# Kernel optimization log

Measured on AMD Instinct MI355X. Metric: run time of the kernel, lower is better.

## Reference

```python
import jax, jax.numpy as jnp
import numpy as np

B, T, H = 1024, 256, 128

def _gru(x, Wx, Wh, b):
    # Keras GRU (reset_after=True), gate order z, r, h. x: [B,T,D], b: [2,3H]
    xp = x @ Wx + b[0]                      # [B,T,3H]
    h0 = jnp.zeros((x.shape[0], Wh.shape[0]), x.dtype)
    def step(h, xt):
        hp = h @ Wh + b[1]
        xz, xr, xh = jnp.split(xt, 3, axis=-1)
        hz, hr, hn = jnp.split(hp, 3, axis=-1)
        z = jax.nn.sigmoid(xz + hz)
        r = jax.nn.sigmoid(xr + hr)
        hh = jnp.tanh(xh + r * hn)
        return z * h + (1.0 - z) * hh, None
    h, _ = jax.lax.scan(step, h0, jnp.swapaxes(xp, 0, 1))
    return h                                 # [B,H]

def setup_inputs() -> dict:
    key = jax.random.key(0)
    ks = jax.random.split(key, 32)
    def gp(k, shape, scale=0.05):
        return (jax.random.normal(k, shape, dtype=jnp.float32) * scale)
    inp = {
        "spatial": jax.random.normal(ks[0], (B, T, 2), dtype=jnp.float32),
        "hour_idx": jax.random.randint(ks[1], (B, T), 0, 24, dtype=jnp.int32),
        "week_idx": jax.random.randint(ks[2], (B, T), 0, 7, dtype=jnp.int32),
        "E_time": gp(ks[3], (24, H)),
        "E_week": gp(ks[4], (7, H)),
        # spatial GRU (input dim 2)
        "Ws_x": gp(ks[5], (2, 3 * H)), "Ws_h": gp(ks[6], (H, 3 * H)), "bs": gp(ks[7], (2, 3 * H)),
        # hour temporal GRU (input dim 128)
        "Wh_x": gp(ks[8], (H, 3 * H)), "Wh_h": gp(ks[9], (H, 3 * H)), "bh": gp(ks[10], (2, 3 * H)),
        # week temporal GRU (input dim 128)
        "Ww_x": gp(ks[11], (H, 3 * H)), "Ww_h": gp(ks[12], (H, 3 * H)), "bw": gp(ks[13], (2, 3 * H)),
        # attention Dense(3) over the channel axis of size 3
        "Wa": gp(ks[14], (3, 3)), "ba": gp(ks[15], (3,)),
        # MLP
        "W1": gp(ks[16], (H, 1024)), "b1": gp(ks[17], (1024,)),
        "W2": gp(ks[18], (1024, 512)), "b2": gp(ks[19], (512,)),
        "W3": gp(ks[20], (512, 256)), "b3": gp(ks[21], (256,)),
        "W4": gp(ks[22], (256, H)), "b4": gp(ks[23], (H,)),
        "Wo": gp(ks[24], (H, 1)), "bo": gp(ks[25], (1,)),
    }
    return inp

def reference(spatial, hour_idx, week_idx, E_time, E_week,
              Ws_x, Ws_h, bs, Wh_x, Wh_h, bh, Ww_x, Ww_h, bw,
              Wa, ba, W1, b1, W2, b2, W3, b3, W4, b4, Wo, bo):
    te = E_time[hour_idx]                    # [B,T,128] gather
    we = E_week[week_idx]                    # [B,T,128] gather
    fs = _gru(spatial, Ws_x, Ws_h, bs)       # [B,128]
    fh = _gru(te, Wh_x, Wh_h, bh)            # [B,128]
    fw = _gru(we, Ww_x, Ww_h, bw)            # [B,128]
    allf = jnp.stack([fs, fh, fw], axis=-1)  # [B,128,3]
    scores = jax.nn.softmax(jax.nn.relu(allf @ Wa + ba), axis=-1)
    sf = jnp.sum(allf * scores, axis=-1)     # [B,128] attention-fused features
    x = jax.nn.relu(sf @ W1 + b1)
    x = jax.nn.relu(x @ W2 + b2)
    x = jax.nn.relu(x @ W3 + b3)
    x = jax.nn.relu(x @ W4 + b4)
    out = (x + sf) @ Wo + bo                 # residual then Dense(1)
    return out[:, 0]                         # [B]
```

## Files before the change

### kernel.cpp

```cpp
#include <hip/hip_runtime.h>
#include <hip/hip_bf16.h>

typedef __attribute__((ext_vector_type(8))) short short8;
typedef __attribute__((ext_vector_type(4))) float f32x4;
typedef __attribute__((ext_vector_type(2))) float f32x2;

#define LOG2E  1.44269504088896340736f
#define NLOG2E (-1.44269504088896340736f)
#define TLOG2E (2.88539008177792681472f)

__device__ __forceinline__ unsigned short f2bf(float f) {
  unsigned u = __builtin_bit_cast(unsigned, f);
  u += 0x7fffu + ((u >> 16) & 1u);
  return (unsigned short)(u >> 16);
}

__global__ void setup_kernel(
    const float* __restrict__ E_time, const float* __restrict__ E_week,
    const float* __restrict__ Wh_x, const float* __restrict__ bh,
    const float* __restrict__ Ww_x, const float* __restrict__ bw,
    const float* __restrict__ W1, const float* __restrict__ W2,
    const float* __restrict__ W3, const float* __restrict__ W4,
    float* __restrict__ Ptime, float* __restrict__ Pweek,
    unsigned short* __restrict__ Wt)
{
  const int b = blockIdx.x;
  const int tid = threadIdx.x;
  if (b < 31) {
    const int c = tid;
    if (b < 24) {
      float acc = bh[c];
      for (int d = 0; d < 128; ++d)
        acc = fmaf(E_time[b * 128 + d], Wh_x[d * 384 + c], acc);
      Ptime[b * 384 + c] = acc;
    } else {
      const int r = b - 24;
      float acc = bw[c];
      for (int d = 0; d < 128; ++d)
        acc = fmaf(E_week[r * 128 + d], Ww_x[d * 384 + c], acc);
      Pweek[r * 384 + c] = acc;
    }
    return;
  }
  const int id = (b - 31) * 384 + tid;
  if (id >= 819200) return;
  if (id < 131072) {
    const int n = id >> 7, k = id & 127;
    Wt[id] = f2bf(W1[k * 1024 + n]);
  } else if (id < 655360) {
    const int off = id - 131072, n = off >> 10, k = off & 1023;
    Wt[id] = f2bf(W2[k * 512 + n]);
  } else if (id < 786432) {
    const int off = id - 655360, n = off >> 9, k = off & 511;
    Wt[id] = f2bf(W3[k * 256 + n]);
  } else {
    const int off = id - 786432, n = off >> 8, k = off & 255;
    Wt[id] = f2bf(W4[k * 128 + n]);
  }
}

__global__ __launch_bounds__(512) void gru_kernel(
    const float* __restrict__ spatial,
    const int* __restrict__ hour_idx,
    const int* __restrict__ week_idx,
    const float* __restrict__ Ws_x,
    const float* __restrict__ Ws_h, const float* __restrict__ bs,
    const float* __restrict__ Wh_h, const float* __restrict__ bh,
    const float* __restrict__ Ww_h, const float* __restrict__ bw,
    const float* __restrict__ Ptime, const float* __restrict__ Pweek,
    float* __restrict__ fs, float* __restrict__ fh, float* __restrict__ fw)
{
  __shared__ __align__(16) unsigned short h_bf[2][16 * 136];
  __shared__ __align__(16) float ptab3[24 * 387 + 1];
  __shared__ __align__(16) float xsp[256 * 16 * 2];
  __shared__ __align__(16) unsigned char idx8[256 * 16];

  const int tid  = threadIdx.x;
  const int lane = tid & 63;
  const int wv   = tid >> 6;
  const int ar   = lane & 15;
  const int akg  = lane >> 4;
  const int gid  = blockIdx.x;
  const int gru  = gid >> 6;
  const int row0 = (gid & 63) * 16;

  const float* __restrict__ Wh   = (gru == 0) ? Ws_h : (gru == 1) ? Wh_h : Ww_h;
  const float* __restrict__ bvec = (gru == 0) ? bs   : (gru == 1) ? bh   : bw;
  float* __restrict__ fout       = (gru == 0) ? fs   : (gru == 1) ? fh   : fw;

  const int j = wv * 16 + ar;
  const float gsc[3] = {NLOG2E, NLOG2E, TLOG2E};

  short8 wfrag[3][4];
  #pragma unroll
  for (int g = 0; g < 3; ++g) {
    const int n = g * 128 + j;
    #pragma unroll
    for (int ks = 0; ks < 4; ++ks) {
      const int k0 = ks * 32 + akg * 8;
      short8 f;
      #pragma unroll
      for (int q = 0; q < 8; ++q)
        f[q] = (short)f2bf(Wh[(k0 + q) * 384 + n] * gsc[g]);
      wfrag[g][ks] = f;
    }
  }

  const float bz = bvec[384 +       j] * NLOG2E;
  const float br = bvec[384 + 128 + j] * NLOG2E;
  const float bn = bvec[384 + 256 + j] * TLOG2E;

  float w0g[3] = {0, 0, 0}, w1g[3] = {0, 0, 0}, b0g[3] = {0, 0, 0};
  if (gru == 0) {
    #pragma unroll
    for (int g = 0; g < 3; ++g) {
      w0g[g] = Ws_x[      g * 128 + j] * gsc[g];
      w1g[g] = Ws_x[384 + g * 128 + j] * gsc[g];
      b0g[g] = bvec[      g * 128 + j] * gsc[g];
    }
  }

  if (gru == 0) {
    for (int e = tid; e < 16 * 256; e += 512) {
      const int i = e >> 8, t = e & 255;
      const f32x2 v = *(const f32x2*)&spatial[((row0 + i) * 256 + t) * 2];
      *(f32x2*)&xsp[(t * 16 + i) * 2] = v;
    }
  } else {
    const int* __restrict__ idxg = (gru == 1) ? hour_idx : week_idx;
    for (int e = tid; e < 16 * 256; e += 512) {
      const int i = e >> 8, t = e & 255;
      idx8[t * 16 + i] = (unsigned char)idxg[(row0 + i) * 256 + t];
    }
    const float* __restrict__ P = (gru == 1) ? Ptime : Pweek;
    const int nr = (gru == 1) ? 24 : 7;
    for (int e = tid; e < nr * 384; e += 512) {
      const int ix = e / 384, c = e - ix * 384;
      const int g = c >> 7, jj = c & 127;
      ptab3[ix * 387 + jj * 3 + g] = P[e] * gsc[g];
    }
  }
  for (int e = tid; e < 16 * 136; e += 512) h_bf[0][e] = 0;

  auto loadx = [&](int t, float (&xp)[4][3]) {
    if (gru == 0) {
      #pragma unroll
      for (int r2 = 0; r2 < 4; ++r2) {
        const f32x2 s = *(const f32x2*)&xsp[(t * 16 + akg * 4 + r2) * 2];
        #pragma unroll
        for (int g = 0; g < 3; ++g)
          xp[r2][g] = fmaf(s.y, w1g[g], fmaf(s.x, w0g[g], b0g[g]));
      }
    } else {
      const unsigned pk = *(const unsigned*)&idx8[t * 16 + akg * 4];
      #pragma unroll
      for (int r2 = 0; r2 < 4; ++r2) {
        const int ix = (pk >> (8 * r2)) & 255;
        const float* __restrict__ p = &ptab3[ix * 387 + j * 3];
        xp[r2][0] = p[0]; xp[r2][1] = p[1]; xp[r2][2] = p[2];
      }
    }
  };

  __syncthreads();

  float hst[4] = {0.f, 0.f, 0.f, 0.f};
  float xpc[4][3];
  loadx(0, xpc);
  int cur = 0;

  #pragma unroll 2
  for (int t = 0; t < 256; ++t) {
    f32x4 accz = {bz, bz, bz, bz};
    f32x4 accr = {br, br, br, br};
    f32x4 accn = {bn, bn, bn, bn};
    const unsigned short* __restrict__ hb = h_bf[cur];
    #pragma unroll
    for (int ks = 0; ks < 4; ++ks) {
      const short8 a = *(const short8*)&hb[ar * 136 + ks * 32 + akg * 8];
      accz = __builtin_amdgcn_mfma_f32_16x16x32_bf16(a, wfrag[0][ks], accz, 0, 0, 0);
      accr = __builtin_amdgcn_mfma_f32_16x16x32_bf16(a, wfrag[1][ks], accr, 0, 0, 0);
      accn = __builtin_amdgcn_mfma_f32_16x16x32_bf16(a, wfrag[2][ks], accn, 0, 0, 0);
    }

    float xpn[4][3];
    if (t < 255) loadx(t + 1, xpn);

    float hn4[4];
    #pragma unroll
    for (int r2 = 0; r2 < 4; ++r2) {
      const float z  = __builtin_amdgcn_rcpf(1.f + __builtin_amdgcn_exp2f(xpc[r2][0] + accz[r2]));
      const float rr = __builtin_amdgcn_rcpf(1.f + __builtin_amdgcn_exp2f(xpc[r2][1] + accr[r2]));
      const float e  = __builtin_amdgcn_exp2f(fmaf(rr, accn[r2], xpc[r2][2]));
      const float hh = fmaf(-2.f, __builtin_amdgcn_rcpf(e + 1.f), 1.f);
      hn4[r2] = fmaf(z, hst[r2] - hh, hh);
      hst[r2] = hn4[r2];
    }

    unsigned p01, p23;
    asm("v_cvt_pk_bf16_f32 %0, %1, %2" : "=v"(p01) : "v"(hn4[0]), "v"(hn4[1]));
    asm("v_cvt_pk_bf16_f32 %0, %1, %2" : "=v"(p23) : "v"(hn4[2]), "v"(hn4[3]));
    unsigned short* __restrict__ ho = h_bf[cur ^ 1];
    ho[(akg * 4 + 0) * 136 + j] = (unsigned short)(p01 & 0xffffu);
    ho[(akg * 4 + 1) * 136 + j] = (unsigned short)(p01 >> 16);
    ho[(akg * 4 + 2) * 136 + j] = (unsigned short)(p23 & 0xffffu);
    ho[(akg * 4 + 3) * 136 + j] = (unsigned short)(p23 >> 16);

    __syncthreads();
    cur ^= 1;
    #pragma unroll
    for (int r2 = 0; r2 < 4; ++r2) {
      xpc[r2][0] = xpn[r2][0]; xpc[r2][1] = xpn[r2][1]; xpc[r2][2] = xpn[r2][2];
    }
  }

  #pragma unroll
  for (int r2 = 0; r2 < 4; ++r2)
    fout[(row0 + akg * 4 + r2) * 128 + j] = hst[r2];
}

template<int K, int N>
__device__ __forceinline__ void mlp_layer(
    const unsigned short* __restrict__ xin, unsigned short* __restrict__ xout,
    const unsigned short* __restrict__ Wt, const float* __restrict__ bias,
    int lane, int wv, float* __restrict__ foutF)
{
  constexpr int NT = N / 64;
  const int ar  = lane & 15;
  const int akg = lane >> 4;
  f32x4 acc[NT];
  #pragma unroll
  for (int nt = 0; nt < NT; ++nt) acc[nt] = f32x4{0.f, 0.f, 0.f, 0.f};
  for (int ks = 0; ks < K / 32; ++ks) {
    const short8 a = *(const short8*)&xin[ar * 1032 + ks * 32 + akg * 8];
    #pragma unroll
    for (int nt = 0; nt < NT; ++nt) {
      const int n = wv * (N / 4) + nt * 16 + ar;
      const short8 b = *(const short8*)&Wt[n * K + ks * 32 + akg * 8];
      acc[nt] = __builtin_amdgcn_mfma_f32_16x16x32_bf16(a, b, acc[nt], 0, 0, 0);
    }
  }
  const int rbase = akg * 4;
  #pragma unroll
  for (int nt = 0; nt < NT; ++nt) {
    const int n = wv * (N / 4) + nt * 16 + ar;
    const float bv = bias[n];
    #pragma unroll
    for (int q = 0; q < 4; ++q) {
      float v = acc[nt][q] + bv;
      v = fmaxf(v, 0.f);
      xout[(rbase + q) * 1032 + n] = f2bf(v);
      if (foutF) foutF[(rbase + q) * 128 + n] = v;
    }
  }
}

__global__ __launch_bounds__(256) void attn_mlp_kernel(
    const float* __restrict__ fs, const float* __restrict__ fh, const float* __restrict__ fw,
    const float* __restrict__ Wa, const float* __restrict__ ba,
    const unsigned short* __restrict__ Wt,
    const float* __restrict__ b1, const float* __restrict__ b2,
    const float* __restrict__ b3, const float* __restrict__ b4,
    const float* __restrict__ Wo, const float* __restrict__ bo,
    float* __restrict__ out)
{
  __shared__ __align__(16) unsigned short xa[16 * 1032];
  __shared__ __align__(16) unsigned short xb[16 * 1032];
  __shared__ __align__(16) float sf_l[16 * 128];
  __shared__ __align__(16) float x4f[16 * 128];

  const int tid  = threadIdx.x;
  const int lane = tid & 63;
  const int wv   = tid >> 6;
  const int row0 = blockIdx.x * 16;

  {
    const int i  = tid >> 4;
    const int j0 = (tid & 15) * 8;
    float wa[9], bav[3];
    #pragma unroll
    for (int q = 0; q < 9; ++q) wa[q] = Wa[q];
    #pragma unroll
    for (int q = 0; q < 3; ++q) bav[q] = ba[q];
    const int base = (row0 + i) * 128 + j0;
    #pragma unroll
    for (int half = 0; half < 2; ++half) {
      const f32x4 a = *(const f32x4*)&fs[base + half * 4];
      const f32x4 b = *(const f32x4*)&fh[base + half * 4];
      const f32x4 c = *(const f32x4*)&fw[base + half * 4];
      #pragma unroll
      for (int q = 0; q < 4; ++q) {
        const float f0 = a[q], f1 = b[q], f2 = c[q];
        float s0 = f0 * wa[0] + f1 * wa[3] + f2 * wa[6] + bav[0];
        float s1 = f0 * wa[1] + f1 * wa[4] + f2 * wa[7] + bav[1];
        float s2 = f0 * wa[2] + f1 * wa[5] + f2 * wa[8] + bav[2];
        s0 = fmaxf(s0, 0.f); s1 = fmaxf(s1, 0.f); s2 = fmaxf(s2, 0.f);
        const float m  = fmaxf(s0, fmaxf(s1, s2));
        const float e0 = __builtin_amdgcn_exp2f((s0 - m) * LOG2E);
        const float e1 = __builtin_amdgcn_exp2f((s1 - m) * LOG2E);
        const float e2 = __builtin_amdgcn_exp2f((s2 - m) * LOG2E);
        const float inv = __builtin_amdgcn_rcpf(e0 + e1 + e2);
        const float sf  = (f0 * e0 + f1 * e1 + f2 * e2) * inv;
        const int jj = j0 + half * 4 + q;
        sf_l[i * 128 + jj] = sf;
        xa[i * 1032 + jj]  = f2bf(sf);
      }
    }
  }
  __syncthreads();

  mlp_layer<128, 1024>(xa, xb, Wt,          b1, lane, wv, nullptr);
  __syncthreads();
  mlp_layer<1024, 512>(xb, xa, Wt + 131072, b2, lane, wv, nullptr);
  __syncthreads();
  mlp_layer<512,  256>(xa, xb, Wt + 655360, b3, lane, wv, nullptr);
  __syncthreads();
  mlp_layer<256,  128>(xb, xa, Wt + 786432, b4, lane, wv, x4f);
  __syncthreads();

  const int row = tid >> 4;
  const int p   = tid & 15;
  float part = 0.f;
  #pragma unroll
  for (int q = 0; q < 8; ++q) {
    const int jj = p + q * 16;
    part += (x4f[row * 128 + jj] + sf_l[row * 128 + jj]) * Wo[jj];
  }
  #pragma unroll
  for (int off = 8; off > 0; off >>= 1)
    part += __shfl_xor(part, off, 16);
  if (p == 0) out[row0 + row] = part + bo[0];
}

extern "C" void kernel_launch(void* const* d_in, const int* in_sizes, int n_in,
                              void* d_out, int out_size, void* d_ws, size_t ws_size,
                              hipStream_t stream) {
  const float* spatial  = (const float*)d_in[0];
  const int*   hour_idx = (const int*)d_in[1];
  const int*   week_idx = (const int*)d_in[2];
  const float* E_time   = (const float*)d_in[3];
  const float* E_week   = (const float*)d_in[4];
  const float* Ws_x = (const float*)d_in[5];
  const float* Ws_h = (const float*)d_in[6];
  const float* bs   = (const float*)d_in[7];
  const float* Wh_x = (const float*)d_in[8];
  const float* Wh_h = (const float*)d_in[9];
  const float* bh   = (const float*)d_in[10];
  const float* Ww_x = (const float*)d_in[11];
  const float* Ww_h = (const float*)d_in[12];
  const float* bw   = (const float*)d_in[13];
  const float* Wa   = (const float*)d_in[14];
  const float* ba   = (const float*)d_in[15];
  const float* W1   = (const float*)d_in[16];
  const float* b1   = (const float*)d_in[17];
  const float* W2   = (const float*)d_in[18];
  const float* b2   = (const float*)d_in[19];
  const float* W3   = (const float*)d_in[20];
  const float* b3   = (const float*)d_in[21];
  const float* W4   = (const float*)d_in[22];
  const float* b4   = (const float*)d_in[23];
  const float* Wo   = (const float*)d_in[24];
  const float* bo   = (const float*)d_in[25];
  float* out = (float*)d_out;

  float* ws    = (float*)d_ws;
  float* Ptime = ws;
  float* Pweek = Ptime + 9216;
  float* fsb   = Pweek + 2688;
  float* fhb   = fsb + 131072;
  float* fwb   = fhb + 131072;
  unsigned short* Wt = (unsigned short*)(fwb + 131072);

  setup_kernel<<<31 + 2134, 384, 0, stream>>>(E_time, E_week, Wh_x, bh, Ww_x, bw,
      W1, W2, W3, W4, Ptime, Pweek, Wt);
  gru_kernel<<<192, 512, 0, stream>>>(spatial, hour_idx, week_idx, Ws_x,
      Ws_h, bs, Wh_h, bh, Ww_h, bw, Ptime, Pweek, fsb, fhb, fwb);
  attn_mlp_kernel<<<64, 256, 0, stream>>>(fsb, fhb, fwb, Wa, ba, Wt,
      b1, b2, b3, b4, Wo, bo, out);
}
```

Measured before the change: 264.4 us.

## Halve GRU block to 4 waves each owning two hidden-column tiles

```diff
diff --git a/kernel.cpp b/kernel.cpp
--- a/kernel.cpp
+++ b/kernel.cpp
@@ -8,6 +8,9 @@
 #define LOG2E  1.44269504088896340736f
 #define NLOG2E (-1.44269504088896340736f)
 #define TLOG2E (2.88539008177792681472f)
+
+#define HS 152
+#define PS 524
 
 __device__ __forceinline__ unsigned short f2bf(float f) {
   unsigned u = __builtin_bit_cast(unsigned, f);
@@ -59,7 +62,7 @@
   }
 }
 
-__global__ __launch_bounds__(512) void gru_kernel(
+__global__ __launch_bounds__(256, 1) void gru_kernel(
     const float* __restrict__ spatial,
     const int* __restrict__ hour_idx,
     const int* __restrict__ week_idx,
@@ -70,8 +73,8 @@
     const float* __restrict__ Ptime, const float* __restrict__ Pweek,
     float* __restrict__ fs, float* __restrict__ fh, float* __restrict__ fw)
 {
-  __shared__ __align__(16) unsigned short h_bf[2][16 * 136];
-  __shared__ __align__(16) float ptab3[24 * 387 + 1];
+  __shared__ __align__(16) unsigned short h_bf[2][16 * HS];
+  __shared__ __align__(16) float ptab4[24 * PS];
   __shared__ __align__(16) float xsp[256 * 16 * 2];
   __shared__ __align__(16) unsigned char idx8[256 * 16];
 
@@ -88,135 +91,157 @@
   const float* __restrict__ bvec = (gru == 0) ? bs   : (gru == 1) ? bh   : bw;
   float* __restrict__ fout       = (gru == 0) ? fs   : (gru == 1) ? fh   : fw;
 
-  const int j = wv * 16 + ar;
+  const int j1 = wv * 16 + ar;
+  const int j2 = j1 + 64;
   const float gsc[3] = {NLOG2E, NLOG2E, TLOG2E};
 
-  short8 wfrag[3][4];
+  short8 wfrag[3][2][4];
   #pragma unroll
   for (int g = 0; g < 3; ++g) {
-    const int n = g * 128 + j;
-    #pragma unroll
-    for (int ks = 0; ks < 4; ++ks) {
-      const int k0 = ks * 32 + akg * 8;
-      short8 f;
-      #pragma unroll
-      for (int q = 0; q < 8; ++q)
-        f[q] = (short)f2bf(Wh[(k0 + q) * 384 + n] * gsc[g]);
-      wfrag[g][ks] = f;
-    }
-  }
-
-  const float bz = bvec[384 +       j] * NLOG2E;
-  const float br = bvec[384 + 128 + j] * NLOG2E;
-  const float bn = bvec[384 + 256 + j] * TLOG2E;
-
-  float w0g[3] = {0, 0, 0}, w1g[3] = {0, 0, 0}, b0g[3] = {0, 0, 0};
+    #pragma unroll
+    for (int jh = 0; jh < 2; ++jh) {
+      const int n = g * 128 + jh * 64 + j1;
+      #pragma unroll
+      for (int ks = 0; ks < 4; ++ks) {
+        const int k0 = ks * 32 + akg * 8;
+        short8 f;
+        #pragma unroll
+        for (int q = 0; q < 8; ++q)
+          f[q] = (short)f2bf(Wh[(k0 + q) * 384 + n] * gsc[g]);
+        wfrag[g][jh][ks] = f;
+      }
+    }
+  }
+
+  float bacc[3][2];
+  #pragma unroll
+  for (int g = 0; g < 3; ++g) {
+    bacc[g][0] = bvec[384 + g * 128 + j1] * gsc[g];
+    bacc[g][1] = bvec[384 + g * 128 + j2] * gsc[g];
+  }
+
+  float w0g[2][3], w1g[2][3], b0g[2][3];
   if (gru == 0) {
     #pragma unroll
-    for (int g = 0; g < 3; ++g) {
-      w0g[g] = Ws_x[      g * 128 + j] * gsc[g];
-      w1g[g] = Ws_x[384 + g * 128 + j] * gsc[g];
-      b0g[g] = bvec[      g * 128 + j] * gsc[g];
+    for (int jh = 0; jh < 2; ++jh) {
+      const int jj = jh ? j2 : j1;
+      #pragma unroll
+      for (int g = 0; g < 3; ++g) {
+        w0g[jh][g] = Ws_x[      g * 128 + jj] * gsc[g];
+        w1g[jh][g] = Ws_x[384 + g * 128 + jj] * gsc[g];
+        b0g[jh][g] = bvec[      g * 128 + jj] * gsc[g];
+      }
     }
   }
 
   if (gru == 0) {
-    for (int e = tid; e < 16 * 256; e += 512) {
+    for (int e = tid; e < 16 * 256; e += 256) {
       const int i = e >> 8, t = e & 255;
       const f32x2 v = *(const f32x2*)&spatial[((row0 + i) * 256 + t) * 2];
       *(f32x2*)&xsp[(t * 16 + i) * 2] = v;
     }
   } else {
     const int* __restrict__ idxg = (gru == 1) ? hour_idx : week_idx;
-    for (int e = tid; e < 16 * 256; e += 512) {
+    for (int e = tid; e < 16 * 256; e += 256) {
       const int i = e >> 8, t = e & 255;
       idx8[t * 16 + i] = (unsigned char)idxg[(row0 + i) * 256 + t];
     }
     const float* __restrict__ P = (gru == 1) ? Ptime : Pweek;
     const int nr = (gru == 1) ? 24 : 7;
-    for (int e = tid; e < nr * 384; e += 512) {
+    for (int e = tid; e < nr * 384; e += 256) {
       const int ix = e / 384, c = e - ix * 384;
       const int g = c >> 7, jj = c & 127;
-      ptab3[ix * 387 + jj * 3 + g] = P[e] * gsc[g];
-    }
-  }
-  for (int e = tid; e < 16 * 136; e += 512) h_bf[0][e] = 0;
-
-  auto loadx = [&](int t, float (&xp)[4][3]) {
+      ptab4[ix * PS + jj * 4 + g] = P[e] * gsc[g];
+    }
+  }
+  for (int e = tid; e < 16 * HS; e += 256) h_bf[0][e] = 0;
+  __syncthreads();
+
+  float hst[2][4];
+  #pragma unroll
+  for (int jh = 0; jh < 2; ++jh)
+    #pragma unroll
+    for (int r2 = 0; r2 < 4; ++r2) hst[jh][r2] = 0.f;
+
+  const int abase = ar * HS;
+
+  auto step = [&](int t, const unsigned short* __restrict__ hb,
+                  unsigned short* __restrict__ ho) {
+    float xp[4][2][3];
     if (gru == 0) {
       #pragma unroll
       for (int r2 = 0; r2 < 4; ++r2) {
         const f32x2 s = *(const f32x2*)&xsp[(t * 16 + akg * 4 + r2) * 2];
         #pragma unroll
-        for (int g = 0; g < 3; ++g)
-          xp[r2][g] = fmaf(s.y, w1g[g], fmaf(s.x, w0g[g], b0g[g]));
+        for (int jh = 0; jh < 2; ++jh)
+          #pragma unroll
+          for (int g = 0; g < 3; ++g)
+            xp[r2][jh][g] = fmaf(s.y, w1g[jh][g], fmaf(s.x, w0g[jh][g], b0g[jh][g]));
       }
     } else {
       const unsigned pk = *(const unsigned*)&idx8[t * 16 + akg * 4];
       #pragma unroll
       for (int r2 = 0; r2 < 4; ++r2) {
         const int ix = (pk >> (8 * r2)) & 255;
-        const float* __restrict__ p = &ptab3[ix * 387 + j * 3];
-        xp[r2][0] = p[0]; xp[r2][1] = p[1]; xp[r2][2] = p[2];
-      }
-    }
+        const f32x4 v1 = *(const f32x4*)&ptab4[ix * PS + j1 * 4];
+        const f32x4 v2 = *(const f32x4*)&ptab4[ix * PS + j2 * 4];
+        xp[r2][0][0] = v1.x; xp[r2][0][1] = v1.y; xp[r2][0][2] = v1.z;
+        xp[r2][1][0] = v2.x; xp[r2][1][1] = v2.y; xp[r2][1][2] = v2.z;
+      }
+    }
+
+    f32x4 acc[3][2];
+    #pragma unroll
+    for (int g = 0; g < 3; ++g)
+      #pragma unroll
+      for (int jh = 0; jh < 2; ++jh)
+        acc[g][jh] = f32x4{bacc[g][jh], bacc[g][jh], bacc[g][jh], bacc[g][jh]};
+    #pragma unroll
+    for (int ks = 0; ks < 4; ++ks) {
+      const short8 a = *(const short8*)&hb[abase + ks * 32 + akg * 8];
+      #pragma unroll
+      for (int g = 0; g < 3; ++g)
+        #pragma unroll
+        for (int jh = 0; jh < 2; ++jh)
+          acc[g][jh] = __builtin_amdgcn_mfma_f32_16x16x32_bf16(a, wfrag[g][jh][ks], acc[g][jh], 0, 0, 0);
+    }
+
+    #pragma unroll
+    for (int jh = 0; jh < 2; ++jh) {
+      float hn4[4];
+      #pragma unroll
+      for (int r2 = 0; r2 < 4; ++r2) {
+        const float z  = __builtin_amdgcn_rcpf(1.f + __builtin_amdgcn_exp2f(xp[r2][jh][0] + acc[0][jh][r2]));
+        const float rr = __builtin_amdgcn_rcpf(1.f + __builtin_amdgcn_exp2f(xp[r2][jh][1] + acc[1][jh][r2]));
+        const float e  = __builtin_amdgcn_exp2f(fmaf(rr, acc[2][jh][r2], xp[r2][jh][2]));
+        const float hh = fmaf(-2.f, __builtin_amdgcn_rcpf(e + 1.f), 1.f);
+        hn4[r2] = fmaf(z, hst[jh][r2] - hh, hh);
+        hst[jh][r2] = hn4[r2];
+      }
+      unsigned p01, p23;
+      asm("v_cvt_pk_bf16_f32 %0, %1, %2" : "=v"(p01) : "v"(hn4[0]), "v"(hn4[1]));
+      asm("v_cvt_pk_bf16_f32 %0, %1, %2" : "=v"(p23) : "v"(hn4[2]), "v"(hn4[3]));
+      const int jj = jh ? j2 : j1;
+      ho[(akg * 4 + 0) * HS + jj] = (unsigned short)(p01 & 0xffffu);
+      ho[(akg * 4 + 1) * HS + jj] = (unsigned short)(p01 >> 16);
+      ho[(akg * 4 + 2) * HS + jj] = (unsigned short)(p23 & 0xffffu);
+      ho[(akg * 4 + 3) * HS + jj] = (unsigned short)(p23 >> 16);
+    }
+    __syncthreads();
   };
 
-  __syncthreads();
-
-  float hst[4] = {0.f, 0.f, 0.f, 0.f};
-  float xpc[4][3];
-  loadx(0, xpc);
-  int cur = 0;
-
-  #pragma unroll 2
-  for (int t = 0; t < 256; ++t) {
-    f32x4 accz = {bz, bz, bz, bz};
-    f32x4 accr = {br, br, br, br};
-    f32x4 accn = {bn, bn, bn, bn};
-    const unsigned short* __restrict__ hb = h_bf[cur];
-    #pragma unroll
-    for (int ks = 0; ks < 4; ++ks) {
-      const short8 a = *(const short8*)&hb[ar * 136 + ks * 32 + akg * 8];
-      accz = __builtin_amdgcn_mfma_f32_16x16x32_bf16(a, wfrag[0][ks], accz, 0, 0, 0);
-      accr = __builtin_amdgcn_mfma_f32_16x16x32_bf16(a, wfrag[1][ks], accr, 0, 0, 0);
-      accn = __builtin_amdgcn_mfma_f32_16x16x32_bf16(a, wfrag[2][ks], accn, 0, 0, 0);
-    }
-
-    float xpn[4][3];
-    if (t < 255) loadx(t + 1, xpn);
-
-    float hn4[4];
-    #pragma unroll
-    for (int r2 = 0; r2 < 4; ++r2) {
-      const float z  = __builtin_amdgcn_rcpf(1.f + __builtin_amdgcn_exp2f(xpc[r2][0] + accz[r2]));
-      const float rr = __builtin_amdgcn_rcpf(1.f + __builtin_amdgcn_exp2f(xpc[r2][1] + accr[r2]));
-      const float e  = __builtin_amdgcn_exp2f(fmaf(rr, accn[r2], xpc[r2][2]));
-      const float hh = fmaf(-2.f, __builtin_amdgcn_rcpf(e + 1.f), 1.f);
-      hn4[r2] = fmaf(z, hst[r2] - hh, hh);
-      hst[r2] = hn4[r2];
-    }
-
-    unsigned p01, p23;
-    asm("v_cvt_pk_bf16_f32 %0, %1, %2" : "=v"(p01) : "v"(hn4[0]), "v"(hn4[1]));
-    asm("v_cvt_pk_bf16_f32 %0, %1, %2" : "=v"(p23) : "v"(hn4[2]), "v"(hn4[3]));
-    unsigned short* __restrict__ ho = h_bf[cur ^ 1];
-    ho[(akg * 4 + 0) * 136 + j] = (unsigned short)(p01 & 0xffffu);
-    ho[(akg * 4 + 1) * 136 + j] = (unsigned short)(p01 >> 16);
-    ho[(akg * 4 + 2) * 136 + j] = (unsigned short)(p23 & 0xffffu);
-    ho[(akg * 4 + 3) * 136 + j] = (unsigned short)(p23 >> 16);
-
-    __syncthreads();
-    cur ^= 1;
-    #pragma unroll
-    for (int r2 = 0; r2 < 4; ++r2) {
-      xpc[r2][0] = xpn[r2][0]; xpc[r2][1] = xpn[r2][1]; xpc[r2][2] = xpn[r2][2];
-    }
-  }
-
-  #pragma unroll
-  for (int r2 = 0; r2 < 4; ++r2)
-    fout[(row0 + akg * 4 + r2) * 128 + j] = hst[r2];
+  for (int tt = 0; tt < 128; ++tt) {
+    step(2 * tt,     h_bf[0], h_bf[1]);
+    step(2 * tt + 1, h_bf[1], h_bf[0]);
+  }
+
+  #pragma unroll
+  for (int jh = 0; jh < 2; ++jh) {
+    const int jj = jh ? j2 : j1;
+    #pragma unroll
+    for (int r2 = 0; r2 < 4; ++r2)
+      fout[(row0 + akg * 4 + r2) * 128 + jj] = hst[jh][r2];
+  }
 }
 
 template<int K, int N>
@@ -373,7 +398,7 @@
 
   setup_kernel<<<31 + 2134, 384, 0, stream>>>(E_time, E_week, Wh_x, bh, Ww_x, bw,
       W1, W2, W3, W4, Ptime, Pweek, Wt);
-  gru_kernel<<<192, 512, 0, stream>>>(spatial, hour_idx, week_idx, Ws_x,
+  gru_kernel<<<192, 256, 0, stream>>>(spatial, hour_idx, week_idx, Ws_x,
       Ws_h, bs, Wh_h, bh, Ww_h, bw, Ptime, Pweek, fsb, fhb, fwb);
   attn_mlp_kernel<<<64, 256, 0, stream>>>(fsb, fhb, fwb, Wa, ba, Wt,
       b1, b2, b3, b4, Wo, bo, out);
```

Measured after the change: 277.7 us. +5.0%, slower.

## Fold GRU input projection into recurrent MFMA via augmented one-hot K slice

Applied to the files above, without the earlier changes.

```diff
diff --git a/kernel.cpp b/kernel.cpp
--- a/kernel.cpp
+++ b/kernel.cpp
@@ -8,6 +8,8 @@
 #define LOG2E  1.44269504088896340736f
 #define NLOG2E (-1.44269504088896340736f)
 #define TLOG2E (2.88539008177792681472f)
+
+#define HES 168
 
 __device__ __forceinline__ unsigned short f2bf(float f) {
   unsigned u = __builtin_bit_cast(unsigned, f);
@@ -59,7 +61,7 @@
   }
 }
 
-__global__ __launch_bounds__(512) void gru_kernel(
+__global__ __launch_bounds__(512, 2) void gru_kernel(
     const float* __restrict__ spatial,
     const int* __restrict__ hour_idx,
     const int* __restrict__ week_idx,
@@ -70,10 +72,7 @@
     const float* __restrict__ Ptime, const float* __restrict__ Pweek,
     float* __restrict__ fs, float* __restrict__ fh, float* __restrict__ fw)
 {
-  __shared__ __align__(16) unsigned short h_bf[2][16 * 136];
-  __shared__ __align__(16) float ptab3[24 * 387 + 1];
-  __shared__ __align__(16) float xsp[256 * 16 * 2];
-  __shared__ __align__(16) unsigned char idx8[256 * 16];
+  __shared__ __align__(16) unsigned short hx[2][16 * HES];
 
   const int tid  = threadIdx.x;
   const int lane = tid & 63;
@@ -87,136 +86,148 @@
   const float* __restrict__ Wh   = (gru == 0) ? Ws_h : (gru == 1) ? Wh_h : Ww_h;
   const float* __restrict__ bvec = (gru == 0) ? bs   : (gru == 1) ? bh   : bw;
   float* __restrict__ fout       = (gru == 0) ? fs   : (gru == 1) ? fh   : fw;
+  const float* __restrict__ Ptab = (gru == 1) ? Ptime : Pweek;
+  const int* __restrict__ idxg   = (gru == 1) ? hour_idx : week_idx;
+  const int NR = (gru == 1) ? 24 : 7;
 
   const int j = wv * 16 + ar;
-  const float gsc[3] = {NLOG2E, NLOG2E, TLOG2E};
-
-  short8 wfrag[3][4];
-  #pragma unroll
-  for (int g = 0; g < 3; ++g) {
-    const int n = g * 128 + j;
-    #pragma unroll
-    for (int ks = 0; ks < 4; ++ks) {
-      const int k0 = ks * 32 + akg * 8;
+
+  short8 wf[15];
+  #pragma unroll
+  for (int g = 0; g < 2; ++g) {
+    #pragma unroll
+    for (int ks = 0; ks < 5; ++ks) {
       short8 f;
       #pragma unroll
-      for (int q = 0; q < 8; ++q)
-        f[q] = (short)f2bf(Wh[(k0 + q) * 384 + n] * gsc[g]);
-      wfrag[g][ks] = f;
-    }
-  }
-
-  const float bz = bvec[384 +       j] * NLOG2E;
-  const float br = bvec[384 + 128 + j] * NLOG2E;
-  const float bn = bvec[384 + 256 + j] * TLOG2E;
-
-  float w0g[3] = {0, 0, 0}, w1g[3] = {0, 0, 0}, b0g[3] = {0, 0, 0};
-  if (gru == 0) {
-    #pragma unroll
-    for (int g = 0; g < 3; ++g) {
-      w0g[g] = Ws_x[      g * 128 + j] * gsc[g];
-      w1g[g] = Ws_x[384 + g * 128 + j] * gsc[g];
-      b0g[g] = bvec[      g * 128 + j] * gsc[g];
-    }
-  }
-
-  if (gru == 0) {
-    for (int e = tid; e < 16 * 256; e += 512) {
-      const int i = e >> 8, t = e & 255;
-      const f32x2 v = *(const f32x2*)&spatial[((row0 + i) * 256 + t) * 2];
-      *(f32x2*)&xsp[(t * 16 + i) * 2] = v;
-    }
-  } else {
-    const int* __restrict__ idxg = (gru == 1) ? hour_idx : week_idx;
-    for (int e = tid; e < 16 * 256; e += 512) {
-      const int i = e >> 8, t = e & 255;
-      idx8[t * 16 + i] = (unsigned char)idxg[(row0 + i) * 256 + t];
-    }
-    const float* __restrict__ P = (gru == 1) ? Ptime : Pweek;
-    const int nr = (gru == 1) ? 24 : 7;
-    for (int e = tid; e < nr * 384; e += 512) {
-      const int ix = e / 384, c = e - ix * 384;
-      const int g = c >> 7, jj = c & 127;
-      ptab3[ix * 387 + jj * 3 + g] = P[e] * gsc[g];
-    }
-  }
-  for (int e = tid; e < 16 * 136; e += 512) h_bf[0][e] = 0;
-
-  auto loadx = [&](int t, float (&xp)[4][3]) {
+      for (int q = 0; q < 8; ++q) {
+        const int k = ks * 32 + akg * 8 + q;
+        float v;
+        if (k < 128) v = Wh[k * 384 + g * 128 + j];
+        else {
+          const int p = k - 128;
+          if (gru == 0) v = (p == 0) ? Ws_x[g * 128 + j]
+                          : (p == 1) ? Ws_x[384 + g * 128 + j] : 0.f;
+          else          v = (p < NR) ? Ptab[p * 384 + g * 128 + j] : 0.f;
+        }
+        f[q] = (short)f2bf(v * NLOG2E);
+      }
+      wf[g * 5 + ks] = f;
+    }
+  }
+  #pragma unroll
+  for (int ks = 0; ks < 4; ++ks) {
+    short8 f;
+    #pragma unroll
+    for (int q = 0; q < 8; ++q) {
+      const int k = ks * 32 + akg * 8 + q;
+      f[q] = (short)f2bf(Wh[k * 384 + 256 + j] * TLOG2E);
+    }
+    wf[10 + ks] = f;
+  }
+  {
+    short8 f;
+    #pragma unroll
+    for (int q = 0; q < 8; ++q) {
+      const int p = akg * 8 + q;
+      float v;
+      if (gru == 0) v = (p == 0) ? Ws_x[256 + j]
+                      : (p == 1) ? Ws_x[384 + 256 + j] : 0.f;
+      else          v = (p < NR) ? Ptab[p * 384 + 256 + j] : 0.f;
+      f[q] = (short)f2bf(v * TLOG2E);
+    }
+    wf[14] = f;
+  }
+
+  const float bz  = (bvec[384 + j]       + (gru == 0 ? bvec[j]       : 0.f)) * NLOG2E;
+  const float br  = (bvec[384 + 128 + j] + (gru == 0 ? bvec[128 + j] : 0.f)) * NLOG2E;
+  const float bnh = bvec[384 + 256 + j] * TLOG2E;
+  const float bnx = (gru == 0 ? bvec[256 + j] : 0.f) * TLOG2E;
+
+  for (int e = tid; e < 2 * 16 * HES; e += 512) ((unsigned short*)hx)[e] = 0;
+  __syncthreads();
+
+  const bool mt  = (tid & 31) == 0;
+  const int mrow = tid >> 5;
+  int ix_prev = 0, ix_cur = 0;
+  if (mt) {
     if (gru == 0) {
-      #pragma unroll
-      for (int r2 = 0; r2 < 4; ++r2) {
-        const f32x2 s = *(const f32x2*)&xsp[(t * 16 + akg * 4 + r2) * 2];
-        #pragma unroll
-        for (int g = 0; g < 3; ++g)
-          xp[r2][g] = fmaf(s.y, w1g[g], fmaf(s.x, w0g[g], b0g[g]));
+      const f32x2 s = *(const f32x2*)&spatial[(row0 + mrow) * 512];
+      unsigned pk;
+      asm("v_cvt_pk_bf16_f32 %0, %1, %2" : "=v"(pk) : "v"(s.x), "v"(s.y));
+      *(unsigned*)&hx[0][mrow * HES + 128] = pk;
+    } else {
+      ix_cur = idxg[(row0 + mrow) * 256];
+      hx[0][mrow * HES + 128 + ix_cur] = 0x3F80;
+    }
+  }
+  __syncthreads();
+
+  float hst[4] = {0.f, 0.f, 0.f, 0.f};
+
+  for (int t = 0; t < 256; ++t) {
+    const unsigned short* __restrict__ hb = hx[t & 1];
+    unsigned short* __restrict__ ho       = hx[(t + 1) & 1];
+
+    short8 a[5];
+    #pragma unroll
+    for (int ks = 0; ks < 5; ++ks)
+      a[ks] = *(const short8*)&hb[ar * HES + ks * 32 + akg * 8];
+
+    f32x2 msp = {0.f, 0.f};
+    int ix_next = 0;
+    const bool mact = mt && (t + 1 < 256);
+    if (mact) {
+      if (gru == 0) msp = *(const f32x2*)&spatial[(row0 + mrow) * 512 + 2 * (t + 1)];
+      else          ix_next = idxg[(row0 + mrow) * 256 + t + 1];
+    }
+
+    f32x4 az  = {bz, bz, bz, bz};
+    f32x4 arr = {br, br, br, br};
+    f32x4 anh = {bnh, bnh, bnh, bnh};
+    f32x4 anx = {bnx, bnx, bnx, bnx};
+    #pragma unroll
+    for (int ks = 0; ks < 4; ++ks) {
+      az  = __builtin_amdgcn_mfma_f32_16x16x32_bf16(a[ks], wf[ks],      az,  0, 0, 0);
+      arr = __builtin_amdgcn_mfma_f32_16x16x32_bf16(a[ks], wf[5 + ks],  arr, 0, 0, 0);
+      anh = __builtin_amdgcn_mfma_f32_16x16x32_bf16(a[ks], wf[10 + ks], anh, 0, 0, 0);
+    }
+    az  = __builtin_amdgcn_mfma_f32_16x16x32_bf16(a[4], wf[4],  az,  0, 0, 0);
+    arr = __builtin_amdgcn_mfma_f32_16x16x32_bf16(a[4], wf[9],  arr, 0, 0, 0);
+    anx = __builtin_amdgcn_mfma_f32_16x16x32_bf16(a[4], wf[14], anx, 0, 0, 0);
+
+    if (mact) {
+      if (gru == 0) {
+        unsigned pk;
+        asm("v_cvt_pk_bf16_f32 %0, %1, %2" : "=v"(pk) : "v"(msp.x), "v"(msp.y));
+        *(unsigned*)&ho[mrow * HES + 128] = pk;
+      } else {
+        if (t >= 1) ho[mrow * HES + 128 + ix_prev] = 0;
+        ho[mrow * HES + 128 + ix_next] = 0x3F80;
+        ix_prev = ix_cur; ix_cur = ix_next;
       }
-    } else {
-      const unsigned pk = *(const unsigned*)&idx8[t * 16 + akg * 4];
-      #pragma unroll
-      for (int r2 = 0; r2 < 4; ++r2) {
-        const int ix = (pk >> (8 * r2)) & 255;
-        const float* __restrict__ p = &ptab3[ix * 387 + j * 3];
-        xp[r2][0] = p[0]; xp[r2][1] = p[1]; xp[r2][2] = p[2];
-      }
-    }
-  };
-
-  __syncthreads();
-
-  float hst[4] = {0.f, 0.f, 0.f, 0.f};
-  float xpc[4][3];
-  loadx(0, xpc);
-  int cur = 0;
-
-  #pragma unroll 2
-  for (int t = 0; t < 256; ++t) {
-    f32x4 accz = {bz, bz, bz, bz};
-    f32x4 accr = {br, br, br, br};
-    f32x4 accn = {bn, bn, bn, bn};
-    const unsigned short* __restrict__ hb = h_bf[cur];
-    #pragma unroll
-    for (int ks = 0; ks < 4; ++ks) {
-      const short8 a = *(const short8*)&hb[ar * 136 + ks * 32 + akg * 8];
-      accz = __builtin_amdgcn_mfma_f32_16x16x32_bf16(a, wfrag[0][ks], accz, 0, 0, 0);
-      accr = __builtin_amdgcn_mfma_f32_16x16x32_bf16(a, wfrag[1][ks], accr, 0, 0, 0);
-      accn = __builtin_amdgcn_mfma_f32_16x16x32_bf16(a, wfrag[2][ks], accn, 0, 0, 0);
-    }
-
-    float xpn[4][3];
-    if (t < 255) loadx(t + 1, xpn);
+    }
 
     float hn4[4];
     #pragma unroll
-    for (int r2 = 0; r2 < 4; ++r2) {
-      const float z  = __builtin_amdgcn_rcpf(1.f + __builtin_amdgcn_exp2f(xpc[r2][0] + accz[r2]));
-      const float rr = __builtin_amdgcn_rcpf(1.f + __builtin_amdgcn_exp2f(xpc[r2][1] + accr[r2]));
-      const float e  = __builtin_amdgcn_exp2f(fmaf(rr, accn[r2], xpc[r2][2]));
+    for (int q = 0; q < 4; ++q) {
+      const float z  = __builtin_amdgcn_rcpf(1.f + __builtin_amdgcn_exp2f(az[q]));
+      const float r  = __builtin_amdgcn_rcpf(1.f + __builtin_amdgcn_exp2f(arr[q]));
+      const float e  = __builtin_amdgcn_exp2f(fmaf(r, anh[q], anx[q]));
       const float hh = fmaf(-2.f, __builtin_amdgcn_rcpf(e + 1.f), 1.f);
-      hn4[r2] = fmaf(z, hst[r2] - hh, hh);
-      hst[r2] = hn4[r2];
-    }
-
-    unsigned p01, p23;
-    asm("v_cvt_pk_bf16_f32 %0, %1, %2" : "=v"(p01) : "v"(hn4[0]), "v"(hn4[1]));
-    asm("v_cvt_pk_bf16_f32 %0, %1, %2" : "=v"(p23) : "v"(hn4[2]), "v"(hn4[3]));
-    unsigned short* __restrict__ ho = h_bf[cur ^ 1];
-    ho[(akg * 4 + 0) * 136 + j] = (unsigned short)(p01 & 0xffffu);
-    ho[(akg * 4 + 1) * 136 + j] = (unsigned short)(p01 >> 16);
-    ho[(akg * 4 + 2) * 136 + j] = (unsigned short)(p23 & 0xffffu);
-    ho[(akg * 4 + 3) * 136 + j] = (unsigned short)(p23 >> 16);
+      hn4[q] = fmaf(z, hst[q] - hh, hh);
+      hst[q] = hn4[q];
+    }
+
+    #pragma unroll
+    for (int q = 0; q < 4; ++q)
+      ho[(akg * 4 + q) * HES + j] = f2bf(hn4[q]);
 
     __syncthreads();
-    cur ^= 1;
-    #pragma unroll
-    for (int r2 = 0; r2 < 4; ++r2) {
-      xpc[r2][0] = xpn[r2][0]; xpc[r2][1] = xpn[r2][1]; xpc[r2][2] = xpn[r2][2];
-    }
-  }
-
-  #pragma unroll
-  for (int r2 = 0; r2 < 4; ++r2)
-    fout[(row0 + akg * 4 + r2) * 128 + j] = hst[r2];
+  }
+
+  #pragma unroll
+  for (int q = 0; q < 4; ++q)
+    fout[(row0 + akg * 4 + q) * 128 + j] = hst[q];
 }
 
 template<int K, int N>
```

Result: faster. 240.7 us (-9.0%).
